# Performance work log

Hardware: AMD Instinct MI355X
Metric: run time of the kernel (lower is better)

The kernel has to match this reference:

```python
import jax, jax.numpy as jnp
import numpy as np

B, C = 1024, 256
GRID_H, GRID_W, PAD_H, PAD_W = 11, 15, 13, 17  # 165 hexes, padded 13x17

def _build_convinds():
    off0 = np.array([-17, -16, -1, 0, 1, 17, 18])
    off1 = np.array([-18, -17, -1, 0, 1, 16, 17])
    inds = np.zeros((GRID_H, GRID_W, 7), dtype=np.int32)
    for y in range(1, GRID_H + 1):
        for x in range(1, GRID_W + 1):
            off = off0 if y % 2 == 0 else off1
            inds[y - 1, x - 1] = off + (y * PAD_W + x)
    return jnp.asarray(inds.reshape(-1))  # (165*7,)

CONVINDS = _build_convinds()

def hexconv(x, W, b):
    # x: (B, 165, C); W: (7C, C); b: (C,)
    bsz = x.shape[0]
    c = x.shape[-1]
    padded = jnp.zeros((bsz, PAD_H, PAD_W, c), x.dtype)
    padded = padded.at[:, 1:1 + GRID_H, 1:1 + GRID_W, :].set(x.reshape(bsz, GRID_H, GRID_W, c))
    padded = padded.reshape(bsz, PAD_H * PAD_W, c)
    gathered = padded[:, CONVINDS, :].reshape(bsz, GRID_H * GRID_W, 7 * c)  # (B,165,7C)
    return gathered @ W + b

def leaky(v):
    return jax.nn.leaky_relu(v, negative_slope=0.01)

def setup_inputs() -> dict:
    key = jax.random.key(0)
    k1, k2, k3, k4, k5 = jax.random.split(key, 5)
    scale = 1.0 / np.sqrt(7 * C)
    return {
        "x": jax.random.normal(k1, (B, 165, C), dtype=jnp.float32),
        "W1": jax.random.uniform(k2, (7 * C, C), jnp.float32, -scale, scale),
        "b1": jax.random.uniform(k3, (C,), jnp.float32, -scale, scale),
        "W2": jax.random.uniform(k4, (7 * C, C), jnp.float32, -scale, scale),
        "b2": jax.random.uniform(k5, (C,), jnp.float32, -scale, scale),
    }

def reference(x, W1, b1, W2, b2):
    # depth=1 residual block: x = act(conv2(act(conv1(x))) + x)
    h = leaky(hexconv(x, W1, b1))
    return leaky(hexconv(h, W2, b2) + x)
```

## Files before the change

kernel.cpp:

```cpp
#include <hip/hip_runtime.h>

typedef __attribute__((ext_vector_type(8))) short short8;
typedef __attribute__((ext_vector_type(4))) float f32x4;

typedef __attribute__((address_space(1))) const unsigned int guint;
typedef __attribute__((address_space(3))) unsigned int luint;

__device__ __forceinline__ void gload16(const void* g, void* l) {
    __builtin_amdgcn_global_load_lds((guint*)g, (luint*)l, 16, 0, 0);
}

__device__ __forceinline__ unsigned short f2bf(float f) {
    unsigned u = __float_as_uint(f);
    u += 0x7fffu + ((u >> 16) & 1u);
    return (unsigned short)(u >> 16);
}

__global__ void __launch_bounds__(256) cvt_x_kernel(const float* __restrict__ in,
                                                    unsigned short* __restrict__ out,
                                                    int n8) {
    int stride = gridDim.x * blockDim.x;
    for (int i = blockIdx.x * blockDim.x + threadIdx.x; i < n8; i += stride) {
        const float4* p = reinterpret_cast<const float4*>(in) + (size_t)i * 2;
        float4 a = p[0], b = p[1];
        short8 o;
        o[0] = (short)f2bf(a.x); o[1] = (short)f2bf(a.y);
        o[2] = (short)f2bf(a.z); o[3] = (short)f2bf(a.w);
        o[4] = (short)f2bf(b.x); o[5] = (short)f2bf(b.y);
        o[6] = (short)f2bf(b.z); o[7] = (short)f2bf(b.w);
        *reinterpret_cast<short8*>(out + (size_t)i * 8) = o;
    }
}

__global__ void __launch_bounds__(256) cvt_wt_kernel(const float* __restrict__ W1,
                                                     const float* __restrict__ W2,
                                                     unsigned short* __restrict__ W1t,
                                                     unsigned short* __restrict__ W2t) {
    const float* W = blockIdx.z ? W2 : W1;
    unsigned short* Wt = blockIdx.z ? W2t : W1t;
    int k0 = blockIdx.x * 64;
    int n0 = blockIdx.y * 64;
    __shared__ float tile[64][65];
    for (int e = threadIdx.x; e < 4096; e += 256) {
        int r = e >> 6, c = e & 63;
        tile[r][c] = W[(size_t)(k0 + r) * 256 + n0 + c];
    }
    __syncthreads();
    for (int e = threadIdx.x; e < 4096; e += 256) {
        int r = e >> 6, c = e & 63;
        Wt[(size_t)(n0 + r) * 1792 + k0 + c] = f2bf(tile[c][r]);
    }
}

template <int MODE>
__global__ void __launch_bounds__(256) hexconv_kernel(
        const unsigned short* __restrict__ xg,
        const unsigned short* __restrict__ wt,
        const float* __restrict__ bias,
        const float* __restrict__ resid,
        void* __restrict__ outp,
        const unsigned short* __restrict__ zp)
{
    __shared__ unsigned short As[128 * 64];
    __shared__ unsigned short Bs[128 * 64];

    const int t = threadIdx.x;
    int bid = blockIdx.x;
    int swz = (bid & 7) * 330 + (bid >> 3);
    const int mb = swz >> 1, nb = swz & 1;
    const int lane = t & 63, w = t >> 6;
    const int wr = w >> 1, wc = w & 1;

    int yq[4], xq[4], browq[4], csw[4];
    unsigned short* adst[4];
    unsigned short* bdst[4];
    const unsigned short* wrowp[4];
    const int chunk = t & 7;
#pragma unroll
    for (int q = 0; q < 4; q++) {
        int row = q * 32 + (t >> 3);
        int m = mb * 128 + row;
        int b = m / 165;
        int i = m - b * 165;
        int y = i / 15;
        int x = i - y * 15;
        yq[q] = y; xq[q] = x; browq[q] = m - i;
        csw[q] = ((chunk ^ (row & 7)) * 8);
        adst[q] = As + (q * 256 + t) * 8;
        bdst[q] = Bs + (q * 256 + t) * 8;
        wrowp[q] = wt + (size_t)(nb * 128 + row) * 1792 + csw[q];
    }

    int offA[4][2], offB[4][2];
    {
        int rA = wr * 64 + (lane & 15);
        int rB = wc * 64 + (lane & 15);
        int r7 = lane & 7;
        int lhi = lane >> 4;
#pragma unroll
        for (int f = 0; f < 4; f++) {
#pragma unroll
            for (int ks = 0; ks < 2; ks++) {
                int gc = ks * 4 + lhi;
                offA[f][ks] = (rA + f * 16) * 64 + ((gc ^ r7) * 8);
                offB[f][ks] = (rB + f * 16) * 64 + ((gc ^ r7) * 8);
            }
        }
    }

    f32x4 acc[4][4];
#pragma unroll
    for (int mi = 0; mi < 4; mi++)
#pragma unroll
        for (int ni = 0; ni < 4; ni++) {
            f32x4 z = {0.f, 0.f, 0.f, 0.f};
            acc[mi][ni] = z;
        }

    const int DY[7]  = {-1, -1, 0, 0, 0, 1, 1};
    const int DXO[7] = { 0,  1, -1, 0, 1, 0, 1};
    const int DXE[7] = {-1,  0, -1, 0, 1, -1, 0};

#pragma unroll 1
    for (int j = 0; j < 7; j++) {
        int aoff[4];
#pragma unroll
        for (int q = 0; q < 4; q++) {
            int dy = DY[j];
            int dx = (yq[q] & 1) ? DXO[j] : DXE[j];
            int ny = yq[q] + dy, nx = xq[q] + dx;
            bool valid = ((unsigned)ny < 11u) && ((unsigned)nx < 15u);
            aoff[q] = valid ? ((browq[q] + ny * 15 + nx) * 256 + csw[q]) : -1;
        }
#pragma unroll 1
        for (int cb = 0; cb < 4; cb++) {
            const int kt = j * 4 + cb;
#pragma unroll
            for (int q = 0; q < 4; q++) {
                const unsigned short* g = (aoff[q] >= 0) ? (xg + aoff[q] + cb * 64) : zp;
                gload16(g, adst[q]);
            }
#pragma unroll
            for (int q = 0; q < 4; q++) {
                gload16(wrowp[q] + kt * 64, bdst[q]);
            }
            __syncthreads();
#pragma unroll
            for (int ks = 0; ks < 2; ks++) {
                short8 av[4], bv[4];
#pragma unroll
                for (int f = 0; f < 4; f++) {
                    av[f] = *reinterpret_cast<const short8*>(&As[offA[f][ks]]);
                    bv[f] = *reinterpret_cast<const short8*>(&Bs[offB[f][ks]]);
                }
#pragma unroll
                for (int mi = 0; mi < 4; mi++)
#pragma unroll
                    for (int ni = 0; ni < 4; ni++)
                        acc[mi][ni] = __builtin_amdgcn_mfma_f32_16x16x32_bf16(
                            av[mi], bv[ni], acc[mi][ni], 0, 0, 0);
            }
            __syncthreads();
        }
    }

    const int colBase = nb * 128 + wc * 64 + (lane & 15);
    const int mrow0 = mb * 128 + wr * 64 + ((lane >> 4) * 4);
    if (MODE == 0) {
        unsigned short* outh = (unsigned short*)outp;
#pragma unroll
        for (int ni = 0; ni < 4; ni++) {
            int col = colBase + ni * 16;
            float bb = bias[col];
#pragma unroll
            for (int mi = 0; mi < 4; mi++) {
                int mr = mrow0 + mi * 16;
#pragma unroll
                for (int r = 0; r < 4; r++) {
                    float v = acc[mi][ni][r] + bb;
                    v = v > 0.f ? v : 0.01f * v;
                    outh[(size_t)(mr + r) * 256 + col] = f2bf(v);
                }
            }
        }
    } else {
        float* outf = (float*)outp;
#pragma unroll
        for (int ni = 0; ni < 4; ni++) {
            int col = colBase + ni * 16;
            float bb = bias[col];
#pragma unroll
            for (int mi = 0; mi < 4; mi++) {
                int mr = mrow0 + mi * 16;
#pragma unroll
                for (int r = 0; r < 4; r++) {
                    float v = acc[mi][ni][r] + bb + resid[(size_t)(mr + r) * 256 + col];
                    v = v > 0.f ? v : 0.01f * v;
                    outf[(size_t)(mr + r) * 256 + col] = v;
                }
            }
        }
    }
}

extern "C" void kernel_launch(void* const* d_in, const int* in_sizes, int n_in,
                              void* d_out, int out_size, void* d_ws, size_t ws_size,
                              hipStream_t stream) {
    const float* x  = (const float*)d_in[0];
    const float* W1 = (const float*)d_in[1];
    const float* b1 = (const float*)d_in[2];
    const float* W2 = (const float*)d_in[3];
    const float* b2 = (const float*)d_in[4];
    float* out = (float*)d_out;

    const size_t XBF = (size_t)1024 * 165 * 256 * 2;
    const size_t WTB = (size_t)256 * 1792 * 2;
    char* ws = (char*)d_ws;
    unsigned short* zp  = (unsigned short*)ws;
    unsigned short* xbf = (unsigned short*)(ws + 256);
    unsigned short* hbf = (unsigned short*)(ws + 256 + XBF);
    unsigned short* w1t = (unsigned short*)(ws + 256 + 2 * XBF);
    unsigned short* w2t = (unsigned short*)(ws + 256 + 2 * XBF + WTB);

    hipMemsetAsync(d_ws, 0, 256, stream);
    cvt_x_kernel<<<2048, 256, 0, stream>>>(x, xbf, 5406720);
    cvt_wt_kernel<<<dim3(28, 4, 2), 256, 0, stream>>>(W1, W2, w1t, w2t);
    hexconv_kernel<0><<<2640, 256, 0, stream>>>(xbf, w1t, b1, nullptr, (void*)hbf, zp);
    hexconv_kernel<1><<<2640, 256, 0, stream>>>(hbf, w2t, b2, x, (void*)out, zp);
}
```

Baseline: 463.2 us.

## Use 256x256 tiles with double-buffered LDS and interleaved MFMA/load scheduling

Replaces the 128x128, 256-thread hex-conv GEMM with a 512-thread kernel that computes a full 256-row by 256-column output tile, so each A gather is reused across all output channels. LDS is double-buffered (128 KB), and the next tile's global-to-LDS loads are staged between quarter-tile MFMA groups, using explicit barriers, lgkmcnt waits and s_setprio to overlap memory with compute. The residual in the second conv is now read from the bf16 copy of x instead of the fp32 input, which halves that read traffic but adds rounding error. The large LDS footprint probably limits occupancy to one block per CU, and 660 blocks leave a partial final wave.

New measurement: 450.6 us. 2.7% less time.

```diff
diff --git a/kernel.cpp b/kernel.cpp
--- a/kernel.cpp
+++ b/kernel.cpp
@@ -15,6 +15,13 @@
     u += 0x7fffu + ((u >> 16) & 1u);
     return (unsigned short)(u >> 16);
 }
+__device__ __forceinline__ float bf2f(unsigned short s) {
+    return __uint_as_float((unsigned)s << 16);
+}
+
+__device__ const int g_DY[7]  = {-1, -1, 0, 0, 0, 1, 1};
+__device__ const int g_DXO[7] = { 0,  1, -1, 0, 1, 0, 1};
+__device__ const int g_DXE[7] = {-1,  0, -1, 0, 1, -1, 0};
 
 __global__ void __launch_bounds__(256) cvt_x_kernel(const float* __restrict__ in,
                                                     unsigned short* __restrict__ out,
@@ -53,152 +60,181 @@
 }
 
 template <int MODE>
-__global__ void __launch_bounds__(256) hexconv_kernel(
+__global__ void __launch_bounds__(512, 2) hexconv8_kernel(
         const unsigned short* __restrict__ xg,
         const unsigned short* __restrict__ wt,
         const float* __restrict__ bias,
-        const float* __restrict__ resid,
+        const unsigned short* __restrict__ residbf,
         void* __restrict__ outp,
         const unsigned short* __restrict__ zp)
 {
-    __shared__ unsigned short As[128 * 64];
-    __shared__ unsigned short Bs[128 * 64];
+    __shared__ unsigned short smem[65536];
 
     const int t = threadIdx.x;
+    const int lane = t & 63, w = t >> 6;
+    const int wr = w >> 2, wc = w & 3;
+
     int bid = blockIdx.x;
-    int swz = (bid & 7) * 330 + (bid >> 3);
-    const int mb = swz >> 1, nb = swz & 1;
-    const int lane = t & 63, w = t >> 6;
-    const int wr = w >> 1, wc = w & 1;
-
-    int yq[4], xq[4], browq[4], csw[4];
-    unsigned short* adst[4];
-    unsigned short* bdst[4];
-    const unsigned short* wrowp[4];
+    int xcd = bid & 7, idx = bid >> 3;
+    const int mb = (xcd < 4 ? xcd * 83 : 332 + (xcd - 4) * 82) + idx;
+
+    const int trow = t >> 3;
     const int chunk = t & 7;
-#pragma unroll
-    for (int q = 0; q < 4; q++) {
-        int row = q * 32 + (t >> 3);
-        int m = mb * 128 + row;
+    const int aswz = (chunk ^ (trow & 7)) * 8;
+    int yv[4], xv[4], brow[4], aoff[4];
+    const unsigned short* wsrcp[4];
+#pragma unroll
+    for (int i = 0; i < 4; ++i) {
+        int row = i * 64 + trow;
+        int m = mb * 256 + row;
         int b = m / 165;
-        int i = m - b * 165;
-        int y = i / 15;
-        int x = i - y * 15;
-        yq[q] = y; xq[q] = x; browq[q] = m - i;
-        csw[q] = ((chunk ^ (row & 7)) * 8);
-        adst[q] = As + (q * 256 + t) * 8;
-        bdst[q] = Bs + (q * 256 + t) * 8;
-        wrowp[q] = wt + (size_t)(nb * 128 + row) * 1792 + csw[q];
-    }
-
-    int offA[4][2], offB[4][2];
+        int ii = m - b * 165;
+        int y = ii / 15;
+        int x = ii - y * 15;
+        yv[i] = y; xv[i] = x; brow[i] = m - ii;
+        wsrcp[i] = wt + (size_t)row * 1792 + aswz;
+    }
+
+#define CALC_AOFF(J) do {                                                     \
+        int dy_ = g_DY[J];                                                    \
+        int dxo_ = g_DXO[J], dxe_ = g_DXE[J];                                 \
+        _Pragma("unroll")                                                     \
+        for (int i = 0; i < 4; ++i) {                                         \
+            int dx_ = (yv[i] & 1) ? dxo_ : dxe_;                              \
+            int ny_ = yv[i] + dy_, nx_ = xv[i] + dx_;                         \
+            bool v_ = ((unsigned)ny_ < 11u) && ((unsigned)nx_ < 15u);         \
+            aoff[i] = v_ ? ((brow[i] + ny_ * 15 + nx_) * 256 + aswz) : -1;    \
+        } } while (0)
+
+    int offA[4][2], offB[2][2][2];
     {
-        int rA = wr * 64 + (lane & 15);
-        int rB = wc * 64 + (lane & 15);
-        int r7 = lane & 7;
-        int lhi = lane >> 4;
-#pragma unroll
-        for (int f = 0; f < 4; f++) {
-#pragma unroll
-            for (int ks = 0; ks < 2; ks++) {
-                int gc = ks * 4 + lhi;
-                offA[f][ks] = (rA + f * 16) * 64 + ((gc ^ r7) * 8);
-                offB[f][ks] = (rB + f * 16) * 64 + ((gc ^ r7) * 8);
-            }
+        int l15 = lane & 15, lhi = lane >> 4, l7 = lane & 7;
+#pragma unroll
+        for (int f = 0; f < 4; ++f)
+#pragma unroll
+            for (int ks = 0; ks < 2; ++ks)
+                offA[f][ks] = (wr * 128 + f * 16 + l15) * 64 + (((ks * 4 + lhi) ^ l7) * 8);
+#pragma unroll
+        for (int nh = 0; nh < 2; ++nh)
+#pragma unroll
+            for (int g = 0; g < 2; ++g)
+#pragma unroll
+                for (int ks = 0; ks < 2; ++ks)
+                    offB[nh][g][ks] = (wc * 64 + nh * 32 + g * 16 + l15) * 64 +
+                                      (((ks * 4 + lhi) ^ l7) * 8);
+    }
+
+    f32x4 acc[8][4];
+#pragma unroll
+    for (int mf = 0; mf < 8; ++mf)
+#pragma unroll
+        for (int nf = 0; nf < 4; ++nf) {
+            f32x4 z = {0.f, 0.f, 0.f, 0.f};
+            acc[mf][nf] = z;
         }
-    }
-
-    f32x4 acc[4][4];
-#pragma unroll
-    for (int mi = 0; mi < 4; mi++)
-#pragma unroll
-        for (int ni = 0; ni < 4; ni++) {
-            f32x4 z = {0.f, 0.f, 0.f, 0.f};
-            acc[mi][ni] = z;
-        }
-
-    const int DY[7]  = {-1, -1, 0, 0, 0, 1, 1};
-    const int DXO[7] = { 0,  1, -1, 0, 1, 0, 1};
-    const int DXE[7] = {-1,  0, -1, 0, 1, -1, 0};
+    short8 a[4][2], b0[2][2], b1[2][2];
+
+#define STAGE_A(TT, P) do {                                                   \
+        int c0_ = ((TT) & 3) * 64;                                            \
+        _Pragma("unroll")                                                     \
+        for (int i = 0; i < 4; ++i) {                                         \
+            const unsigned short* g_ = (aoff[i] >= 0) ? (xg + aoff[i] + c0_) : zp; \
+            gload16(g_, &smem[(P) * 32768 + i * 4096 + t * 8]);               \
+        } } while (0)
+#define STAGE_B(TT, P) do {                                                   \
+        int ko_ = (TT) * 64;                                                  \
+        _Pragma("unroll")                                                     \
+        for (int i = 0; i < 4; ++i)                                           \
+            gload16(wsrcp[i] + ko_, &smem[(P) * 32768 + 16384 + i * 4096 + t * 8]); \
+        } while (0)
+
+#define LDA(P, MH) do { _Pragma("unroll") for (int f = 0; f < 4; ++f)         \
+        _Pragma("unroll") for (int ks = 0; ks < 2; ++ks)                      \
+            a[f][ks] = *(const short8*)&smem[(P) * 32768 + (MH) * 4096 + offA[f][ks]]; \
+        } while (0)
+#define LDB(P, NH, DST) do { _Pragma("unroll") for (int g = 0; g < 2; ++g)    \
+        _Pragma("unroll") for (int ks = 0; ks < 2; ++ks)                      \
+            DST[g][ks] = *(const short8*)&smem[(P) * 32768 + 16384 + offB[NH][g][ks]]; \
+        } while (0)
+
+#define QUAD(MH, NH, BF) do { _Pragma("unroll") for (int f = 0; f < 4; ++f)   \
+        _Pragma("unroll") for (int g = 0; g < 2; ++g)                         \
+        _Pragma("unroll") for (int ks = 0; ks < 2; ++ks)                      \
+            acc[(MH) * 4 + f][(NH) * 2 + g] = __builtin_amdgcn_mfma_f32_16x16x32_bf16( \
+                a[f][ks], BF[g][ks], acc[(MH) * 4 + f][(NH) * 2 + g], 0, 0, 0); \
+        } while (0)
+
+#define BAR() __builtin_amdgcn_s_barrier()
+#define LGKM0() do { asm volatile("s_waitcnt lgkmcnt(0)" ::: "memory");       \
+                     __builtin_amdgcn_sched_barrier(0); } while (0)
+#define VM0() asm volatile("s_waitcnt vmcnt(0)" ::: "memory")
+#define PRIO(N) __builtin_amdgcn_s_setprio(N)
+
+#define TILE(T28, P) do {                                                     \
+        int tt_ = (T28) + 1;                                                  \
+                                                                      \
+        if (tt_ < 28) {                                                       \
+            if ((tt_ & 3) == 0) { int jn_ = tt_ >> 2; CALC_AOFF(jn_); }       \
+            STAGE_A(tt_, 1 - (P));                                            \
+        }                                                                     \
+        LDA(P, 0); LDB(P, 0, b0);                                             \
+        BAR(); LGKM0(); PRIO(1); QUAD(0, 0, b0); PRIO(0); BAR();              \
+                                                                      \
+        if (tt_ < 28) STAGE_B(tt_, 1 - (P));                                  \
+        LDB(P, 1, b1);                                                        \
+        BAR(); LGKM0(); PRIO(1); QUAD(0, 1, b1); PRIO(0); BAR();              \
+                                                                      \
+        LDA(P, 1);                                                            \
+        BAR(); LGKM0(); PRIO(1); QUAD(1, 1, b1); PRIO(0); BAR();              \
+                                                                      \
+        PRIO(1); QUAD(1, 0, b0); PRIO(0);                                     \
+        VM0(); BAR();                                                         \
+    } while (0)
+
+    CALC_AOFF(0);
+    STAGE_A(0, 0);
+    STAGE_B(0, 0);
+    VM0(); BAR();
 
 #pragma unroll 1
-    for (int j = 0; j < 7; j++) {
-        int aoff[4];
-#pragma unroll
-        for (int q = 0; q < 4; q++) {
-            int dy = DY[j];
-            int dx = (yq[q] & 1) ? DXO[j] : DXE[j];
-            int ny = yq[q] + dy, nx = xq[q] + dx;
-            bool valid = ((unsigned)ny < 11u) && ((unsigned)nx < 15u);
-            aoff[q] = valid ? ((browq[q] + ny * 15 + nx) * 256 + csw[q]) : -1;
-        }
-#pragma unroll 1
-        for (int cb = 0; cb < 4; cb++) {
-            const int kt = j * 4 + cb;
-#pragma unroll
-            for (int q = 0; q < 4; q++) {
-                const unsigned short* g = (aoff[q] >= 0) ? (xg + aoff[q] + cb * 64) : zp;
-                gload16(g, adst[q]);
-            }
-#pragma unroll
-            for (int q = 0; q < 4; q++) {
-                gload16(wrowp[q] + kt * 64, bdst[q]);
-            }
-            __syncthreads();
-#pragma unroll
-            for (int ks = 0; ks < 2; ks++) {
-                short8 av[4], bv[4];
-#pragma unroll
-                for (int f = 0; f < 4; f++) {
-                    av[f] = *reinterpret_cast<const short8*>(&As[offA[f][ks]]);
-                    bv[f] = *reinterpret_cast<const short8*>(&Bs[offB[f][ks]]);
-                }
-#pragma unroll
-                for (int mi = 0; mi < 4; mi++)
-#pragma unroll
-                    for (int ni = 0; ni < 4; ni++)
-                        acc[mi][ni] = __builtin_amdgcn_mfma_f32_16x16x32_bf16(
-                            av[mi], bv[ni], acc[mi][ni], 0, 0, 0);
-            }
-            __syncthreads();
-        }
-    }
-
-    const int colBase = nb * 128 + wc * 64 + (lane & 15);
-    const int mrow0 = mb * 128 + wr * 64 + ((lane >> 4) * 4);
+    for (int it = 0; it < 14; ++it) {
+        TILE(2 * it, 0);
+        TILE(2 * it + 1, 1);
+    }
+
+    const size_t mrowbase = (size_t)mb * 256 + wr * 128;
+    const int l15 = lane & 15, lq = (lane >> 4) * 4;
     if (MODE == 0) {
         unsigned short* outh = (unsigned short*)outp;
 #pragma unroll
-        for (int ni = 0; ni < 4; ni++) {
-            int col = colBase + ni * 16;
+        for (int nf = 0; nf < 4; ++nf) {
+            int col = wc * 64 + nf * 16 + l15;
             float bb = bias[col];
 #pragma unroll
-            for (int mi = 0; mi < 4; mi++) {
-                int mr = mrow0 + mi * 16;
-#pragma unroll
-                for (int r = 0; r < 4; r++) {
-                    float v = acc[mi][ni][r] + bb;
+            for (int mf = 0; mf < 8; ++mf)
+#pragma unroll
+                for (int r = 0; r < 4; ++r) {
+                    size_t mr = mrowbase + mf * 16 + lq + r;
+                    float v = acc[mf][nf][r] + bb;
                     v = v > 0.f ? v : 0.01f * v;
-                    outh[(size_t)(mr + r) * 256 + col] = f2bf(v);
+                    outh[mr * 256 + col] = f2bf(v);
                 }
-            }
         }
     } else {
         float* outf = (float*)outp;
 #pragma unroll
-        for (int ni = 0; ni < 4; ni++) {
-            int col = colBase + ni * 16;
+        for (int nf = 0; nf < 4; ++nf) {
+            int col = wc * 64 + nf * 16 + l15;
             float bb = bias[col];
 #pragma unroll
-            for (int mi = 0; mi < 4; mi++) {
-                int mr = mrow0 + mi * 16;
-#pragma unroll
-                for (int r = 0; r < 4; r++) {
-                    float v = acc[mi][ni][r] + bb + resid[(size_t)(mr + r) * 256 + col];
+            for (int mf = 0; mf < 8; ++mf)
+#pragma unroll
+                for (int r = 0; r < 4; ++r) {
+                    size_t mr = mrowbase + mf * 16 + lq + r;
+                    float v = acc[mf][nf][r] + bb + bf2f(residbf[mr * 256 + col]);
                     v = v > 0.f ? v : 0.01f * v;
-                    outf[(size_t)(mr + r) * 256 + col] = v;
+                    outf[mr * 256 + col] = v;
                 }
-            }
         }
     }
 }
@@ -225,6 +261,6 @@
     hipMemsetAsync(d_ws, 0, 256, stream);
     cvt_x_kernel<<<2048, 256, 0, stream>>>(x, xbf, 5406720);
     cvt_wt_kernel<<<dim3(28, 4, 2), 256, 0, stream>>>(W1, W2, w1t, w2t);
-    hexconv_kernel<0><<<2640, 256, 0, stream>>>(xbf, w1t, b1, nullptr, (void*)hbf, zp);
-    hexconv_kernel<1><<<2640, 256, 0, stream>>>(hbf, w2t, b2, x, (void*)out, zp);
-}
+    hexconv8_kernel<0><<<660, 512, 0, stream>>>(xbf, w1t, b1, nullptr, (void*)hbf, zp);
+    hexconv8_kernel<1><<<660, 512, 0, stream>>>(hbf, w2t, b2, xbf, (void*)out, zp);
+}
```

## Load MFMA operands directly from global into registers, drop LDS staging

Applied to the files above, without the earlier changes.

Replaces the LDS-staged 128x128 GEMM tile with a 256x64 tile in which each wave loads its A (gathered hex neighbours) and B fragments straight from global memory into registers. A triple-buffered A and double-buffered B register prefetch is software-pipelined across a fully unrolled 56-step K loop, and the in-loop barriers are gone. The epilogue goes through LDS so stores are coalesced, and the residual is read from the bf16 copy of x instead of fp32. This removes LDS traffic and synchronisation, but each wave now re-reads B from global/L2 with no sharing, register pressure rises, and the bf16 residual changes numerics slightly.

New measurement: 1.135 ms. 145% more time.

```diff
diff --git a/kernel.cpp b/kernel.cpp
--- a/kernel.cpp
+++ b/kernel.cpp
@@ -2,19 +2,19 @@
 
 typedef __attribute__((ext_vector_type(8))) short short8;
 typedef __attribute__((ext_vector_type(4))) float f32x4;
-
-typedef __attribute__((address_space(1))) const unsigned int guint;
-typedef __attribute__((address_space(3))) unsigned int luint;
-
-__device__ __forceinline__ void gload16(const void* g, void* l) {
-    __builtin_amdgcn_global_load_lds((guint*)g, (luint*)l, 16, 0, 0);
-}
 
 __device__ __forceinline__ unsigned short f2bf(float f) {
     unsigned u = __float_as_uint(f);
     u += 0x7fffu + ((u >> 16) & 1u);
     return (unsigned short)(u >> 16);
 }
+__device__ __forceinline__ float bf2f(unsigned short s) {
+    return __uint_as_float((unsigned)s << 16);
+}
+
+__device__ const int g_DY[7]  = {-1, -1, 0, 0, 0, 1, 1};
+__device__ const int g_DXO[7] = { 0,  1, -1, 0, 1, 0, 1};
+__device__ const int g_DXE[7] = {-1,  0, -1, 0, 1, -1, 0};
 
 __global__ void __launch_bounds__(256) cvt_x_kernel(const float* __restrict__ in,
                                                     unsigned short* __restrict__ out,
@@ -53,152 +53,144 @@
 }
 
 template <int MODE>
-__global__ void __launch_bounds__(256) hexconv_kernel(
+__global__ void __launch_bounds__(256) hexconv_reg_kernel(
         const unsigned short* __restrict__ xg,
         const unsigned short* __restrict__ wt,
         const float* __restrict__ bias,
-        const float* __restrict__ resid,
+        const unsigned short* __restrict__ residbf,
         void* __restrict__ outp,
         const unsigned short* __restrict__ zp)
 {
-    __shared__ unsigned short As[128 * 64];
-    __shared__ unsigned short Bs[128 * 64];
+    __shared__ float tlds[4 * 64 * 68];
 
     const int t = threadIdx.x;
+    const int lane = t & 63, w = t >> 6;
+    const int l15 = lane & 15, lhi = lane >> 4;
+
     int bid = blockIdx.x;
-    int swz = (bid & 7) * 330 + (bid >> 3);
-    const int mb = swz >> 1, nb = swz & 1;
-    const int lane = t & 63, w = t >> 6;
-    const int wr = w >> 1, wc = w & 1;
-
-    int yq[4], xq[4], browq[4], csw[4];
-    unsigned short* adst[4];
-    unsigned short* bdst[4];
-    const unsigned short* wrowp[4];
-    const int chunk = t & 7;
-#pragma unroll
-    for (int q = 0; q < 4; q++) {
-        int row = q * 32 + (t >> 3);
-        int m = mb * 128 + row;
+    int gl = (bid & 7) * 330 + (bid >> 3);
+    const int mb = gl >> 2, nb = gl & 3;
+
+    int yv[4], xv[4], browv[4];
+#pragma unroll
+    for (int f = 0; f < 4; ++f) {
+        int m = mb * 256 + w * 64 + f * 16 + l15;
         int b = m / 165;
         int i = m - b * 165;
         int y = i / 15;
         int x = i - y * 15;
-        yq[q] = y; xq[q] = x; browq[q] = m - i;
-        csw[q] = ((chunk ^ (row & 7)) * 8);
-        adst[q] = As + (q * 256 + t) * 8;
-        bdst[q] = Bs + (q * 256 + t) * 8;
-        wrowp[q] = wt + (size_t)(nb * 128 + row) * 1792 + csw[q];
-    }
-
-    int offA[4][2], offB[4][2];
-    {
-        int rA = wr * 64 + (lane & 15);
-        int rB = wc * 64 + (lane & 15);
-        int r7 = lane & 7;
-        int lhi = lane >> 4;
-#pragma unroll
-        for (int f = 0; f < 4; f++) {
-#pragma unroll
-            for (int ks = 0; ks < 2; ks++) {
-                int gc = ks * 4 + lhi;
-                offA[f][ks] = (rA + f * 16) * 64 + ((gc ^ r7) * 8);
-                offB[f][ks] = (rB + f * 16) * 64 + ((gc ^ r7) * 8);
+        yv[f] = y; xv[f] = x; browv[f] = m - i;
+    }
+
+    const unsigned short* bbase[4];
+#pragma unroll
+    for (int f = 0; f < 4; ++f)
+        bbase[f] = wt + (size_t)(nb * 64 + f * 16 + l15) * 1792 + lhi * 8;
+
+    f32x4 acc[4][4];
+#pragma unroll
+    for (int f = 0; f < 4; ++f)
+#pragma unroll
+        for (int g = 0; g < 4; ++g) {
+            f32x4 z = {0.f, 0.f, 0.f, 0.f};
+            acc[f][g] = z;
+        }
+
+    const unsigned short* abase[2][4];
+    short8 ab[3][4], bb[2][4];
+
+#define SET_ABASE(SET, J) do {                                                \
+        const int dy_ = g_DY[J], dxo_ = g_DXO[J], dxe_ = g_DXE[J];            \
+        _Pragma("unroll")                                                     \
+        for (int f = 0; f < 4; ++f) {                                         \
+            int dx_ = (yv[f] & 1) ? dxo_ : dxe_;                              \
+            int ny_ = yv[f] + dy_, nx_ = xv[f] + dx_;                         \
+            bool v_ = ((unsigned)ny_ < 11u) && ((unsigned)nx_ < 15u);         \
+            abase[SET][f] = v_ ? (xg + (size_t)(browv[f] + ny_ * 15 + nx_) * 256 + lhi * 8) \
+                               : zp;                                          \
+        } } while (0)
+
+#define LOADA(DST, SET, S) do { _Pragma("unroll")                             \
+        for (int f = 0; f < 4; ++f)                                           \
+            DST[f] = *(const short8*)(abase[SET][f] + (S) * 32); } while (0)
+#define LOADB(DST, SS) do { _Pragma("unroll")                                 \
+        for (int f = 0; f < 4; ++f)                                           \
+            DST[f] = *(const short8*)(bbase[f] + (SS) * 32); } while (0)
+
+#define STEP(AB, BB) do { _Pragma("unroll")                                   \
+        for (int f = 0; f < 4; ++f) _Pragma("unroll")                         \
+        for (int g = 0; g < 4; ++g)                                           \
+            acc[f][g] = __builtin_amdgcn_mfma_f32_16x16x32_bf16(              \
+                AB[f], BB[g], acc[f][g], 0, 0, 0); } while (0)
+
+    SET_ABASE(0, 0);
+    LOADA(ab[0], 0, 0);
+    LOADA(ab[1], 0, 1);
+    LOADB(bb[0], 0);
+
+#pragma unroll
+    for (int ss = 0; ss < 56; ++ss) {
+        const int pa = ss + 2, pj = pa >> 3, ps = pa & 7;
+        if (pa < 56) {
+            if (ps == 0) SET_ABASE(pj & 1, pj);
+            LOADA(ab[pa % 3], pj & 1, ps);
+        }
+        if (ss + 1 < 56) LOADB(bb[(ss + 1) & 1], ss + 1);
+        STEP(ab[ss % 3], bb[ss & 1]);
+    }
+
+    float* my = tlds + w * (64 * 68);
+#pragma unroll
+    for (int g = 0; g < 4; ++g) {
+        float bz = bias[nb * 64 + g * 16 + l15];
+#pragma unroll
+        for (int f = 0; f < 4; ++f)
+#pragma unroll
+            for (int r = 0; r < 4; ++r) {
+                float v = acc[f][g][r] + bz;
+                if (MODE == 0) v = v > 0.f ? v : 0.01f * v;
+                my[(f * 16 + lhi * 4 + r) * 68 + g * 16 + l15] = v;
             }
-        }
-    }
-
-    f32x4 acc[4][4];
-#pragma unroll
-    for (int mi = 0; mi < 4; mi++)
-#pragma unroll
-        for (int ni = 0; ni < 4; ni++) {
-            f32x4 z = {0.f, 0.f, 0.f, 0.f};
-            acc[mi][ni] = z;
-        }
-
-    const int DY[7]  = {-1, -1, 0, 0, 0, 1, 1};
-    const int DXO[7] = { 0,  1, -1, 0, 1, 0, 1};
-    const int DXE[7] = {-1,  0, -1, 0, 1, -1, 0};
-
-#pragma unroll 1
-    for (int j = 0; j < 7; j++) {
-        int aoff[4];
-#pragma unroll
-        for (int q = 0; q < 4; q++) {
-            int dy = DY[j];
-            int dx = (yq[q] & 1) ? DXO[j] : DXE[j];
-            int ny = yq[q] + dy, nx = xq[q] + dx;
-            bool valid = ((unsigned)ny < 11u) && ((unsigned)nx < 15u);
-            aoff[q] = valid ? ((browq[q] + ny * 15 + nx) * 256 + csw[q]) : -1;
-        }
-#pragma unroll 1
-        for (int cb = 0; cb < 4; cb++) {
-            const int kt = j * 4 + cb;
-#pragma unroll
-            for (int q = 0; q < 4; q++) {
-                const unsigned short* g = (aoff[q] >= 0) ? (xg + aoff[q] + cb * 64) : zp;
-                gload16(g, adst[q]);
-            }
-#pragma unroll
-            for (int q = 0; q < 4; q++) {
-                gload16(wrowp[q] + kt * 64, bdst[q]);
-            }
-            __syncthreads();
-#pragma unroll
-            for (int ks = 0; ks < 2; ks++) {
-                short8 av[4], bv[4];
-#pragma unroll
-                for (int f = 0; f < 4; f++) {
-                    av[f] = *reinterpret_cast<const short8*>(&As[offA[f][ks]]);
-                    bv[f] = *reinterpret_cast<const short8*>(&Bs[offB[f][ks]]);
-                }
-#pragma unroll
-                for (int mi = 0; mi < 4; mi++)
-#pragma unroll
-                    for (int ni = 0; ni < 4; ni++)
-                        acc[mi][ni] = __builtin_amdgcn_mfma_f32_16x16x32_bf16(
-                            av[mi], bv[ni], acc[mi][ni], 0, 0, 0);
-            }
-            __syncthreads();
-        }
-    }
-
-    const int colBase = nb * 128 + wc * 64 + (lane & 15);
-    const int mrow0 = mb * 128 + wr * 64 + ((lane >> 4) * 4);
-    if (MODE == 0) {
-        unsigned short* outh = (unsigned short*)outp;
-#pragma unroll
-        for (int ni = 0; ni < 4; ni++) {
-            int col = colBase + ni * 16;
-            float bb = bias[col];
-#pragma unroll
-            for (int mi = 0; mi < 4; mi++) {
-                int mr = mrow0 + mi * 16;
-#pragma unroll
-                for (int r = 0; r < 4; r++) {
-                    float v = acc[mi][ni][r] + bb;
-                    v = v > 0.f ? v : 0.01f * v;
-                    outh[(size_t)(mr + r) * 256 + col] = f2bf(v);
-                }
-            }
-        }
-    } else {
-        float* outf = (float*)outp;
-#pragma unroll
-        for (int ni = 0; ni < 4; ni++) {
-            int col = colBase + ni * 16;
-            float bb = bias[col];
-#pragma unroll
-            for (int mi = 0; mi < 4; mi++) {
-                int mr = mrow0 + mi * 16;
-#pragma unroll
-                for (int r = 0; r < 4; r++) {
-                    float v = acc[mi][ni][r] + bb + resid[(size_t)(mr + r) * 256 + col];
-                    v = v > 0.f ? v : 0.01f * v;
-                    outf[(size_t)(mr + r) * 256 + col] = v;
-                }
-            }
+    }
+    __syncthreads();
+    const int rrow = lane >> 3, rc8 = (lane & 7) * 8;
+#pragma unroll
+    for (int rr = 0; rr < 8; ++rr) {
+        int row = rr * 8 + rrow;
+        float4 v0 = *(float4*)&my[row * 68 + rc8];
+        float4 v1 = *(float4*)&my[row * 68 + rc8 + 4];
+        size_t gm = (size_t)mb * 256 + w * 64 + row;
+        int gc = nb * 64 + rc8;
+        if (MODE == 0) {
+            unsigned short* outh = (unsigned short*)outp;
+            short8 o;
+            o[0] = (short)f2bf(v0.x); o[1] = (short)f2bf(v0.y);
+            o[2] = (short)f2bf(v0.z); o[3] = (short)f2bf(v0.w);
+            o[4] = (short)f2bf(v1.x); o[5] = (short)f2bf(v1.y);
+            o[6] = (short)f2bf(v1.z); o[7] = (short)f2bf(v1.w);
+            *(short8*)&outh[gm * 256 + gc] = o;
+        } else {
+            float* outf = (float*)outp;
+            short8 rv = *(const short8*)&residbf[gm * 256 + gc];
+            float4 w0, w1;
+            w0.x = v0.x + bf2f((unsigned short)rv[0]);
+            w0.y = v0.y + bf2f((unsigned short)rv[1]);
+            w0.z = v0.z + bf2f((unsigned short)rv[2]);
+            w0.w = v0.w + bf2f((unsigned short)rv[3]);
+            w1.x = v1.x + bf2f((unsigned short)rv[4]);
+            w1.y = v1.y + bf2f((unsigned short)rv[5]);
+            w1.z = v1.z + bf2f((unsigned short)rv[6]);
+            w1.w = v1.w + bf2f((unsigned short)rv[7]);
+            w0.x = w0.x > 0.f ? w0.x : 0.01f * w0.x;
+            w0.y = w0.y > 0.f ? w0.y : 0.01f * w0.y;
+            w0.z = w0.z > 0.f ? w0.z : 0.01f * w0.z;
+            w0.w = w0.w > 0.f ? w0.w : 0.01f * w0.w;
+            w1.x = w1.x > 0.f ? w1.x : 0.01f * w1.x;
+            w1.y = w1.y > 0.f ? w1.y : 0.01f * w1.y;
+            w1.z = w1.z > 0.f ? w1.z : 0.01f * w1.z;
+            w1.w = w1.w > 0.f ? w1.w : 0.01f * w1.w;
+            *(float4*)&outf[gm * 256 + gc] = w0;
+            *(float4*)&outf[gm * 256 + gc + 4] = w1;
         }
     }
 }
@@ -217,14 +209,14 @@
     const size_t WTB = (size_t)256 * 1792 * 2;
     char* ws = (char*)d_ws;
     unsigned short* zp  = (unsigned short*)ws;
-    unsigned short* xbf = (unsigned short*)(ws + 256);
-    unsigned short* hbf = (unsigned short*)(ws + 256 + XBF);
-    unsigned short* w1t = (unsigned short*)(ws + 256 + 2 * XBF);
-    unsigned short* w2t = (unsigned short*)(ws + 256 + 2 * XBF + WTB);
-
-    hipMemsetAsync(d_ws, 0, 256, stream);
+    unsigned short* xbf = (unsigned short*)(ws + 512);
+    unsigned short* hbf = (unsigned short*)(ws + 512 + XBF);
+    unsigned short* w1t = (unsigned short*)(ws + 512 + 2 * XBF);
+    unsigned short* w2t = (unsigned short*)(ws + 512 + 2 * XBF + WTB);
+
+    hipMemsetAsync(d_ws, 0, 512, stream);
     cvt_x_kernel<<<2048, 256, 0, stream>>>(x, xbf, 5406720);
     cvt_wt_kernel<<<dim3(28, 4, 2), 256, 0, stream>>>(W1, W2, w1t, w2t);
-    hexconv_kernel<0><<<2640, 256, 0, stream>>>(xbf, w1t, b1, nullptr, (void*)hbf, zp);
-    hexconv_kernel<1><<<2640, 256, 0, stream>>>(hbf, w2t, b2, x, (void*)out, zp);
-}
+    hexconv_reg_kernel<0><<<2640, 256, 0, stream>>>(xbf, w1t, b1, nullptr, (void*)hbf, zp);
+    hexconv_reg_kernel<1><<<2640, 256, 0, stream>>>(hbf, w2t, b2, xbf, (void*)out, zp);
+}
```
